# Optimization experiments

Measured on AMD Instinct MI355X. Metric: run time of the kernel, lower is better.

The kernel has to match this reference:

```python
import jax, jax.numpy as jnp
import numpy as np

H = 512   # hidden_size
B = 32    # batch
S = 2048  # src_len
NEG = -1e10


def setup_inputs() -> dict:
    key = jax.random.key(0)
    k1, k2, k3, k4, k5, k6 = jax.random.split(key, 6)
    hidden = jax.random.normal(k1, (B, 2 * H), dtype=jnp.float32)
    encoder_outputs = jax.random.normal(k2, (S, B, 2 * H), dtype=jnp.float32)
    mask = jax.random.randint(k3, (B, S), 0, 2, dtype=jnp.int32)
    # params: nn.Linear(4H, H) -> weight [H, 4H], bias [H]; v ~ U[0,1) [H]
    bound = 1.0 / np.sqrt(4 * H)
    attn_w = jax.random.uniform(k4, (H, 4 * H), minval=-bound, maxval=bound, dtype=jnp.float32)
    attn_b = jax.random.uniform(k5, (H,), minval=-bound, maxval=bound, dtype=jnp.float32)
    v = jax.random.uniform(k6, (H,), dtype=jnp.float32)
    return {"hidden": hidden, "encoder_outputs": encoder_outputs, "mask": mask,
            "attn_w": attn_w, "attn_b": attn_b, "v": v}


def reference(hidden, encoder_outputs, mask, attn_w, attn_b, v):
    # hidden: [B, 2H] -> [B, S, 2H]; encoder_outputs: [S, B, 2H] -> [B, S, 2H]
    src_len = encoder_outputs.shape[0]
    h = jnp.broadcast_to(hidden[:, None, :], (hidden.shape[0], src_len, hidden.shape[1]))
    eo = jnp.transpose(encoder_outputs, (1, 0, 2))
    cat = jnp.concatenate((h, eo), axis=2)                      # [B, S, 4H]
    energy = jnp.tanh(jnp.einsum('bsf,hf->bsh', cat, attn_w) + attn_b)  # [B, S, H]
    attention = jnp.einsum('bsh,h->bs', energy, v)              # [B, S]
    attention = jnp.where(mask == 0, NEG, attention)
    return jax.nn.softmax(attention, axis=1)
```

## Files before the change

kernel.cpp:

```cpp
#include <hip/hip_runtime.h>

#define SLEN 2048
#define BATCH 32
#define HDIM 512
#define KDIM 1024

typedef _Float16 f16x8 __attribute__((ext_vector_type(8)));
typedef _Float16 f16x4 __attribute__((ext_vector_type(4)));
typedef float f32x4 __attribute__((ext_vector_type(4)));

__device__ __forceinline__ void gload16(const void* g, void* l) {
  __builtin_amdgcn_global_load_lds(
      (const __attribute__((address_space(1))) unsigned int*)g,
      (__attribute__((address_space(3))) unsigned int*)l, 16, 0, 0);
}

__device__ __forceinline__ float fast_tanh(float x) {
  float e = __expf(2.0f * x);
  return 1.0f - 2.0f * __builtin_amdgcn_rcpf(e + 1.0f);
}

__global__ __launch_bounds__(256) void prep_k(const float* __restrict__ attn_w,
                                              const float* __restrict__ attn_b,
                                              const float* __restrict__ hidden,
                                              _Float16* __restrict__ Bt,
                                              float* __restrict__ s1,
                                              float* __restrict__ score) {
  if (blockIdx.x < 512) {
    int t = blockIdx.x * 256 + threadIdx.x;
    int h = t >> 8;
    int c = t & 255;
    float4 x = *(const float4*)(attn_w + (size_t)h * 2048 + 1024 + c * 4);
    f16x4 y = {(_Float16)x.x, (_Float16)x.y, (_Float16)x.z, (_Float16)x.w};
    *(f16x4*)(Bt + (size_t)h * 1024 + c * 4) = y;
  } else if (blockIdx.x < 4608) {
    int o = (blockIdx.x - 512) * 4 + (threadIdx.x >> 6);
    int b = o >> 9, h = o & 511;
    int lane = threadIdx.x & 63;
    const float4* hp = (const float4*)(hidden + (size_t)b * 1024);
    const float4* wp = (const float4*)(attn_w + (size_t)h * 2048);
    float acc = 0.f;
#pragma unroll
    for (int c = 0; c < 4; ++c) {
      float4 a = hp[c * 64 + lane];
      float4 wv = wp[c * 64 + lane];
      acc += a.x * wv.x + a.y * wv.y + a.z * wv.z + a.w * wv.w;
    }
#pragma unroll
    for (int off = 1; off < 64; off <<= 1) acc += __shfl_xor(acc, off);
    if (lane == 0) s1[o] = acc + attn_b[h];
  } else {
    int idx = (blockIdx.x - 4608) * 256 + threadIdx.x;
    float4 z = {0.f, 0.f, 0.f, 0.f};
    ((float4*)score)[idx] = z;
    ((float4*)score)[idx + 8192] = z;
  }
}

__global__ __launch_bounds__(256, 2) void gemm_k(const float* __restrict__ eo,
                                                 const _Float16* __restrict__ Bt,
                                                 const float* __restrict__ s1,
                                                 const float* __restrict__ v,
                                                 float* __restrict__ score) {
  constexpr int BK = 64;
  __shared__ __align__(16) float As[256 * BK];
  __shared__ __align__(16) _Float16 Bs[128 * BK];

  int bid = blockIdx.x;
  int x = bid & 7;
  int q = bid >> 3;
  int nt = q & 3;
  int mt = (q >> 2) * 8 + x;

  int tid = threadIdx.x;
  int lane = tid & 63;
  int w = tid >> 6;
  int wm = w * 64;

  const float* ga[8];
  const _Float16* gb[4];
#pragma unroll
  for (int ii = 0; ii < 8; ++ii) {
    int iss = w * 16 + ii;
    int rloc = iss * 4 + (lane >> 4);
    int sc = (lane & 15) ^ (rloc & 15);
    ga[ii] = eo + (size_t)(mt * 256 + rloc) * KDIM + sc * 4;
  }
#pragma unroll
  for (int ii = 0; ii < 4; ++ii) {
    int iss = w * 4 + ii;
    int rloc = iss * 8 + (lane >> 3);
    int sc = (lane & 7) ^ (rloc & 7);
    gb[ii] = Bt + (size_t)(nt * 128 + rloc) * KDIM + sc * 8;
  }

  f32x4 acc[4][8];
#pragma unroll
  for (int i = 0; i < 4; ++i)
#pragma unroll
    for (int j = 0; j < 8; ++j) acc[i][j] = (f32x4){0.f, 0.f, 0.f, 0.f};

  int mrow = lane & 15;
  int quad = lane >> 4;
  for (int kt = 0; kt < KDIM / BK; ++kt) {
    __syncthreads();
#pragma unroll
    for (int ii = 0; ii < 8; ++ii) {
      gload16(ga[ii], (char*)As + (w * 16 + ii) * 1024);
      gload16(ga[ii] + 32 * KDIM, (char*)As + (w * 16 + ii + 8) * 1024);
      ga[ii] += BK;
    }
#pragma unroll
    for (int ii = 0; ii < 4; ++ii) {
      gload16(gb[ii], (char*)Bs + (w * 4 + ii) * 1024);
      gb[ii] += BK;
    }
    __syncthreads();

#pragma unroll
    for (int kk = 0; kk < 2; ++kk) {
      int c0 = kk * 8 + quad * 2;
      int cB = kk * 4 + quad;
      f16x8 af[4], bf[8];
#pragma unroll
      for (int j = 0; j < 8; ++j)
        bf[j] = *(const f16x8*)&Bs[(16 * j + mrow) * BK + ((cB ^ (mrow & 7)) << 3)];
#pragma unroll
      for (int i = 0; i < 4; ++i) {
        const float* pa = &As[(wm + 16 * i + mrow) * BK];
        float4 a0 = *(const float4*)(pa + ((c0 ^ mrow) << 2));
        float4 a1 = *(const float4*)(pa + (((c0 + 1) ^ mrow) << 2));
        f16x8 t = {(_Float16)a0.x, (_Float16)a0.y, (_Float16)a0.z, (_Float16)a0.w,
                   (_Float16)a1.x, (_Float16)a1.y, (_Float16)a1.z, (_Float16)a1.w};
        af[i] = t;
      }
#pragma unroll
      for (int i = 0; i < 4; ++i)
#pragma unroll
        for (int j = 0; j < 8; ++j)
          acc[i][j] = __builtin_amdgcn_mfma_f32_16x16x32_f16(af[i], bf[j], acc[i][j], 0, 0, 0);
    }
  }

  __syncthreads();
  float* s1s = (float*)As;
  float* vsm = (float*)Bs;
  for (int t = tid; t < 1024; t += 256) {
    int bb = t >> 5, cc = t & 31;
    ((float4*)s1s)[bb * 33 + cc] = *(const float4*)(s1 + (size_t)bb * 512 + nt * 128 + cc * 4);
  }
  if (tid < 32) ((float4*)vsm)[tid] = *(const float4*)(v + nt * 128 + tid * 4);
  __syncthreads();

  int lcol = lane & 15;
  float vv[8];
#pragma unroll
  for (int j = 0; j < 8; ++j) vv[j] = vsm[16 * j + lcol];

#pragma unroll
  for (int i = 0; i < 4; ++i) {
#pragma unroll
    for (int r = 0; r < 4; ++r) {
      int mloc = wm + 16 * i + 4 * quad + r;
      int bb = mloc & 31;
      float sum = 0.f;
#pragma unroll
      for (int j = 0; j < 8; ++j) {
        float e = acc[i][j][r] + s1s[bb * 132 + 16 * j + lcol];
        sum += fast_tanh(e) * vv[j];
      }
      sum += __shfl_xor(sum, 1);
      sum += __shfl_xor(sum, 2);
      sum += __shfl_xor(sum, 4);
      sum += __shfl_xor(sum, 8);
      if (lcol == 0) {
        int mg = mt * 256 + mloc;
        atomicAdd(&score[(mg & 31) * SLEN + (mg >> 5)], sum);
      }
    }
  }
}

__global__ __launch_bounds__(256) void softmax_k(const float* __restrict__ score,
                                                 const int* __restrict__ mask,
                                                 float* __restrict__ out) {
  int b = blockIdx.x;
  int tid = threadIdx.x;
  int lane = tid & 63, w = tid >> 6;
  __shared__ float red[8];
  float vals[8];
  float mx = -3.4e38f;
#pragma unroll
  for (int i = 0; i < 8; ++i) {
    int s = i * 256 + tid;
    float xv = score[b * SLEN + s];
    if (mask[b * SLEN + s] == 0) xv = -1e10f;
    vals[i] = xv;
    mx = fmaxf(mx, xv);
  }
#pragma unroll
  for (int off = 1; off < 64; off <<= 1) mx = fmaxf(mx, __shfl_xor(mx, off));
  if (lane == 0) red[w] = mx;
  __syncthreads();
  mx = fmaxf(fmaxf(red[0], red[1]), fmaxf(red[2], red[3]));
  float sum = 0.f;
#pragma unroll
  for (int i = 0; i < 8; ++i) {
    vals[i] = __expf(vals[i] - mx);
    sum += vals[i];
  }
#pragma unroll
  for (int off = 1; off < 64; off <<= 1) sum += __shfl_xor(sum, off);
  if (lane == 0) red[4 + w] = sum;
  __syncthreads();
  sum = red[4] + red[5] + red[6] + red[7];
  float inv = 1.0f / sum;
#pragma unroll
  for (int i = 0; i < 8; ++i) out[b * SLEN + i * 256 + tid] = vals[i] * inv;
}

extern "C" void kernel_launch(void* const* d_in, const int* in_sizes, int n_in,
                              void* d_out, int out_size, void* d_ws, size_t ws_size,
                              hipStream_t stream) {
  const float* hidden = (const float*)d_in[0];
  const float* eo     = (const float*)d_in[1];
  const int*   mask   = (const int*)d_in[2];
  const float* attn_w = (const float*)d_in[3];
  const float* attn_b = (const float*)d_in[4];
  const float* v      = (const float*)d_in[5];
  float* out = (float*)d_out;

  char* wsb = (char*)d_ws;
  _Float16* Bt = (_Float16*)wsb;
  float* s1    = (float*)(wsb + (1 << 20));
  float* score = (float*)(wsb + (1 << 20) + (1 << 16));

  prep_k<<<4640, 256, 0, stream>>>(attn_w, attn_b, hidden, Bt, s1, score);
  gemm_k<<<1024, 256, 0, stream>>>(eo, Bt, s1, v, score);
  softmax_k<<<BATCH, 256, 0, stream>>>(score, mask, out);
}
```

Baseline: 441.2 us.

## Double-buffer GEMM LDS tiles with BK=32 and prefetch the next K tile

Halves the K tile to 32 and keeps two LDS buffers for A and B. The next tile's global-to-LDS loads are issued before the MFMAs on the current tile run, so load latency can overlap compute, and the loop needs one barrier per iteration instead of two. Address swizzles are rebuilt for the narrower tile, and `s_setprio` raises wave priority around the MFMA block. Total LDS use stays about the same. The overlap may be lost if the compiler inserts conservative vmcnt waits before the LDS reads, and the smaller K step doubles the number of loop iterations and barriers.

```diff
diff --git a/kernel.cpp b/kernel.cpp
--- a/kernel.cpp
+++ b/kernel.cpp
@@ -62,9 +62,10 @@
                                                  const float* __restrict__ s1,
                                                  const float* __restrict__ v,
                                                  float* __restrict__ score) {
-  constexpr int BK = 64;
-  __shared__ __align__(16) float As[256 * BK];
-  __shared__ __align__(16) _Float16 Bs[128 * BK];
+  constexpr int BK = 32;
+  constexpr int NKT = KDIM / BK;
+  __shared__ __align__(16) float As[2][256 * BK];
+  __shared__ __align__(16) _Float16 Bs[2][128 * BK];
 
   int bid = blockIdx.x;
   int x = bid & 7;
@@ -78,21 +79,14 @@
   int wm = w * 64;
 
   const float* ga[8];
-  const _Float16* gb[4];
-#pragma unroll
-  for (int ii = 0; ii < 8; ++ii) {
-    int iss = w * 16 + ii;
-    int rloc = iss * 4 + (lane >> 4);
-    int sc = (lane & 15) ^ (rloc & 15);
-    ga[ii] = eo + (size_t)(mt * 256 + rloc) * KDIM + sc * 4;
-  }
-#pragma unroll
-  for (int ii = 0; ii < 4; ++ii) {
-    int iss = w * 4 + ii;
-    int rloc = iss * 8 + (lane >> 3);
-    int sc = (lane & 7) ^ (rloc & 7);
-    gb[ii] = Bt + (size_t)(nt * 128 + rloc) * KDIM + sc * 8;
-  }
+  const _Float16* gb[2];
+#pragma unroll
+  for (int i = 0; i < 8; ++i)
+    ga[i] = eo + (size_t)(mt * 256 + 64 * w + 8 * i + (lane >> 3)) * KDIM
+              + (((lane & 7) ^ (lane >> 3)) << 2);
+  gb[0] = Bt + (size_t)(nt * 128 + 32 * w + (lane >> 2)) * KDIM
+            + (((lane & 3) ^ (lane >> 4)) << 3);
+  gb[1] = gb[0] + 16 * KDIM;
 
   f32x4 acc[4][8];
 #pragma unroll
@@ -102,44 +96,57 @@
 
   int mrow = lane & 15;
   int quad = lane >> 4;
-  for (int kt = 0; kt < KDIM / BK; ++kt) {
+  int bchunk = (quad ^ (mrow >> 2)) & 3;
+  int as_sw = mrow & 7;
+
+  {
+    gload16(gb[0], (char*)Bs[0] + (w * 2 + 0) * 1024);
+    gload16(gb[1], (char*)Bs[0] + (w * 2 + 1) * 1024);
+    gb[0] += BK; gb[1] += BK;
+#pragma unroll
+    for (int i = 0; i < 8; ++i) {
+      gload16(ga[i], (char*)As[0] + (w * 8 + i) * 1024);
+      ga[i] += BK;
+    }
+  }
+
+  for (int kt = 0; kt < NKT; ++kt) {
+    int cur = kt & 1;
     __syncthreads();
-#pragma unroll
-    for (int ii = 0; ii < 8; ++ii) {
-      gload16(ga[ii], (char*)As + (w * 16 + ii) * 1024);
-      gload16(ga[ii] + 32 * KDIM, (char*)As + (w * 16 + ii + 8) * 1024);
-      ga[ii] += BK;
-    }
-#pragma unroll
-    for (int ii = 0; ii < 4; ++ii) {
-      gload16(gb[ii], (char*)Bs + (w * 4 + ii) * 1024);
-      gb[ii] += BK;
-    }
-    __syncthreads();
-
-#pragma unroll
-    for (int kk = 0; kk < 2; ++kk) {
-      int c0 = kk * 8 + quad * 2;
-      int cB = kk * 4 + quad;
-      f16x8 af[4], bf[8];
+
+    if (kt + 1 < NKT) {
+      gload16(gb[0], (char*)Bs[cur ^ 1] + (w * 2 + 0) * 1024);
+      gload16(gb[1], (char*)Bs[cur ^ 1] + (w * 2 + 1) * 1024);
+      gb[0] += BK; gb[1] += BK;
+#pragma unroll
+      for (int i = 0; i < 8; ++i) {
+        gload16(ga[i], (char*)As[cur ^ 1] + (w * 8 + i) * 1024);
+        ga[i] += BK;
+      }
+    }
+
+    const float* Ab = As[cur];
+    const _Float16* Bb = Bs[cur];
+    f16x8 bf[8], af[4];
+#pragma unroll
+    for (int j = 0; j < 8; ++j)
+      bf[j] = *(const f16x8*)&Bb[(16 * j + mrow) * BK + (bchunk << 3)];
+#pragma unroll
+    for (int i = 0; i < 4; ++i) {
+      const float* pa = &Ab[(wm + 16 * i + mrow) * BK];
+      float4 a0 = *(const float4*)(pa + (((2 * quad) ^ as_sw) << 2));
+      float4 a1 = *(const float4*)(pa + (((2 * quad + 1) ^ as_sw) << 2));
+      f16x8 t = {(_Float16)a0.x, (_Float16)a0.y, (_Float16)a0.z, (_Float16)a0.w,
+                 (_Float16)a1.x, (_Float16)a1.y, (_Float16)a1.z, (_Float16)a1.w};
+      af[i] = t;
+    }
+    __builtin_amdgcn_s_setprio(1);
+#pragma unroll
+    for (int i = 0; i < 4; ++i)
 #pragma unroll
       for (int j = 0; j < 8; ++j)
-        bf[j] = *(const f16x8*)&Bs[(16 * j + mrow) * BK + ((cB ^ (mrow & 7)) << 3)];
-#pragma unroll
-      for (int i = 0; i < 4; ++i) {
-        const float* pa = &As[(wm + 16 * i + mrow) * BK];
-        float4 a0 = *(const float4*)(pa + ((c0 ^ mrow) << 2));
-        float4 a1 = *(const float4*)(pa + (((c0 + 1) ^ mrow) << 2));
-        f16x8 t = {(_Float16)a0.x, (_Float16)a0.y, (_Float16)a0.z, (_Float16)a0.w,
-                   (_Float16)a1.x, (_Float16)a1.y, (_Float16)a1.z, (_Float16)a1.w};
-        af[i] = t;
-      }
-#pragma unroll
-      for (int i = 0; i < 4; ++i)
-#pragma unroll
-        for (int j = 0; j < 8; ++j)
-          acc[i][j] = __builtin_amdgcn_mfma_f32_16x16x32_f16(af[i], bf[j], acc[i][j], 0, 0, 0);
-    }
+        acc[i][j] = __builtin_amdgcn_mfma_f32_16x16x32_f16(af[i], bf[j], acc[i][j], 0, 0, 0);
+    __builtin_amdgcn_s_setprio(0);
   }
 
   __syncthreads();
```

New measurement: 439.0 us. No clear change (-0.5%).

## Load A fragments directly from global and stage B halves in large LDS buffer

Applied to the files above, without the earlier changes.

The GEMM kernel now uses 512-thread blocks covering 512 rows by 128 columns. It stages the fp16 weight tile for half of K (512 columns) into a 128KB LDS buffer with XOR swizzling. Encoder-output rows are read straight from global into registers and converted to fp16, which drops the async global-to-LDS copies of the fp32 A tile and most of the per-K-step barriers. In exchange, A loads lose LDS sharing and coalescing and must hide their latency through unrolling. The 128KB of LDS per block with launch_bounds(512,2) also constrains occupancy.

```diff
diff --git a/kernel.cpp b/kernel.cpp
--- a/kernel.cpp
+++ b/kernel.cpp
@@ -8,12 +8,6 @@
 typedef _Float16 f16x8 __attribute__((ext_vector_type(8)));
 typedef _Float16 f16x4 __attribute__((ext_vector_type(4)));
 typedef float f32x4 __attribute__((ext_vector_type(4)));
-
-__device__ __forceinline__ void gload16(const void* g, void* l) {
-  __builtin_amdgcn_global_load_lds(
-      (const __attribute__((address_space(1))) unsigned int*)g,
-      (__attribute__((address_space(3))) unsigned int*)l, 16, 0, 0);
-}
 
 __device__ __forceinline__ float fast_tanh(float x) {
   float e = __expf(2.0f * x);
@@ -57,83 +51,83 @@
   }
 }
 
-__global__ __launch_bounds__(256, 2) void gemm_k(const float* __restrict__ eo,
+__global__ __launch_bounds__(512, 2) void gemm_k(const float* __restrict__ eo,
                                                  const _Float16* __restrict__ Bt,
                                                  const float* __restrict__ s1,
                                                  const float* __restrict__ v,
                                                  float* __restrict__ score) {
-  constexpr int BK = 64;
-  __shared__ __align__(16) float As[256 * BK];
-  __shared__ __align__(16) _Float16 Bs[128 * BK];
+  __shared__ __align__(16) char smem[131072];
 
   int bid = blockIdx.x;
   int x = bid & 7;
-  int q = bid >> 3;
-  int nt = q & 3;
-  int mt = (q >> 2) * 8 + x;
+  int nt = (bid >> 3) & 3;
+  int mt = (bid >> 5) * 8 + x;
 
   int tid = threadIdx.x;
   int lane = tid & 63;
   int w = tid >> 6;
   int wm = w * 64;
-
-  const float* ga[8];
-  const _Float16* gb[4];
-#pragma unroll
-  for (int ii = 0; ii < 8; ++ii) {
-    int iss = w * 16 + ii;
-    int rloc = iss * 4 + (lane >> 4);
-    int sc = (lane & 15) ^ (rloc & 15);
-    ga[ii] = eo + (size_t)(mt * 256 + rloc) * KDIM + sc * 4;
-  }
-#pragma unroll
-  for (int ii = 0; ii < 4; ++ii) {
-    int iss = w * 4 + ii;
-    int rloc = iss * 8 + (lane >> 3);
-    int sc = (lane & 7) ^ (rloc & 7);
-    gb[ii] = Bt + (size_t)(nt * 128 + rloc) * KDIM + sc * 8;
-  }
-
-  f32x4 acc[4][8];
-#pragma unroll
-  for (int i = 0; i < 4; ++i)
-#pragma unroll
-    for (int j = 0; j < 8; ++j) acc[i][j] = (f32x4){0.f, 0.f, 0.f, 0.f};
-
   int mrow = lane & 15;
   int quad = lane >> 4;
-  for (int kt = 0; kt < KDIM / BK; ++kt) {
+  int rk = mrow & 7;
+
+  f32x4 acc[4][8];
+#pragma unroll
+  for (int i = 0; i < 4; ++i)
+#pragma unroll
+    for (int j = 0; j < 8; ++j) acc[i][j] = (f32x4){0.f, 0.f, 0.f, 0.f};
+
+#pragma unroll 1
+  for (int half = 0; half < 2; ++half) {
+    int h0 = half * 512;
+
     __syncthreads();
-#pragma unroll
-    for (int ii = 0; ii < 8; ++ii) {
-      gload16(ga[ii], (char*)As + (w * 16 + ii) * 1024);
-      gload16(ga[ii] + 32 * KDIM, (char*)As + (w * 16 + ii + 8) * 1024);
-      ga[ii] += BK;
-    }
-#pragma unroll
-    for (int ii = 0; ii < 4; ++ii) {
-      gload16(gb[ii], (char*)Bs + (w * 4 + ii) * 1024);
-      gb[ii] += BK;
+    {
+      int r = tid >> 2;
+      int cg = (tid & 3) * 16;
+      const _Float16* src = Bt + (size_t)(nt * 128 + r) * 1024 + h0 + cg * 8;
+      char* dst = smem + r * 1024;
+#pragma unroll
+      for (int c = 0; c < 16; ++c) {
+        f16x8 vd = *(const f16x8*)(src + c * 8);
+        int pc = (cg + c) ^ (r & 7);
+        *(f16x8*)(dst + pc * 16) = vd;
+      }
     }
     __syncthreads();
 
-#pragma unroll
-    for (int kk = 0; kk < 2; ++kk) {
-      int c0 = kk * 8 + quad * 2;
-      int cB = kk * 4 + quad;
-      f16x8 af[4], bf[8];
+    const float* aB0 = eo + (size_t)(mt * 512 + wm + 0  + mrow) * 1024 + h0 + quad * 8;
+    const float* aB1 = eo + (size_t)(mt * 512 + wm + 16 + mrow) * 1024 + h0 + quad * 8;
+    const float* aB2 = eo + (size_t)(mt * 512 + wm + 32 + mrow) * 1024 + h0 + quad * 8;
+    const float* aB3 = eo + (size_t)(mt * 512 + wm + 48 + mrow) * 1024 + h0 + quad * 8;
+
+#pragma unroll 2
+    for (int ks = 0; ks < 16; ++ks) {
+      float4 ar0 = *(const float4*)(aB0 + ks * 32);
+      float4 ar1 = *(const float4*)(aB0 + ks * 32 + 4);
+      float4 ar2 = *(const float4*)(aB1 + ks * 32);
+      float4 ar3 = *(const float4*)(aB1 + ks * 32 + 4);
+      float4 ar4 = *(const float4*)(aB2 + ks * 32);
+      float4 ar5 = *(const float4*)(aB2 + ks * 32 + 4);
+      float4 ar6 = *(const float4*)(aB3 + ks * 32);
+      float4 ar7 = *(const float4*)(aB3 + ks * 32 + 4);
+
+      int cx = ((ks * 4 + quad) ^ rk) << 4;
+      f16x8 bf[8];
 #pragma unroll
       for (int j = 0; j < 8; ++j)
-        bf[j] = *(const f16x8*)&Bs[(16 * j + mrow) * BK + ((cB ^ (mrow & 7)) << 3)];
-#pragma unroll
-      for (int i = 0; i < 4; ++i) {
-        const float* pa = &As[(wm + 16 * i + mrow) * BK];
-        float4 a0 = *(const float4*)(pa + ((c0 ^ mrow) << 2));
-        float4 a1 = *(const float4*)(pa + (((c0 + 1) ^ mrow) << 2));
-        f16x8 t = {(_Float16)a0.x, (_Float16)a0.y, (_Float16)a0.z, (_Float16)a0.w,
-                   (_Float16)a1.x, (_Float16)a1.y, (_Float16)a1.z, (_Float16)a1.w};
-        af[i] = t;
-      }
+        bf[j] = *(const f16x8*)(smem + ((16 * j + mrow) << 10) + cx);
+
+      f16x8 af[4];
+      af[0] = (f16x8){(_Float16)ar0.x, (_Float16)ar0.y, (_Float16)ar0.z, (_Float16)ar0.w,
+                      (_Float16)ar1.x, (_Float16)ar1.y, (_Float16)ar1.z, (_Float16)ar1.w};
+      af[1] = (f16x8){(_Float16)ar2.x, (_Float16)ar2.y, (_Float16)ar2.z, (_Float16)ar2.w,
+                      (_Float16)ar3.x, (_Float16)ar3.y, (_Float16)ar3.z, (_Float16)ar3.w};
+      af[2] = (f16x8){(_Float16)ar4.x, (_Float16)ar4.y, (_Float16)ar4.z, (_Float16)ar4.w,
+                      (_Float16)ar5.x, (_Float16)ar5.y, (_Float16)ar5.z, (_Float16)ar5.w};
+      af[3] = (f16x8){(_Float16)ar6.x, (_Float16)ar6.y, (_Float16)ar6.z, (_Float16)ar6.w,
+                      (_Float16)ar7.x, (_Float16)ar7.y, (_Float16)ar7.z, (_Float16)ar7.w};
+
 #pragma unroll
       for (int i = 0; i < 4; ++i)
 #pragma unroll
@@ -143,16 +137,16 @@
   }
 
   __syncthreads();
-  float* s1s = (float*)As;
-  float* vsm = (float*)Bs;
-  for (int t = tid; t < 1024; t += 256) {
+  float* s1s = (float*)smem;
+  float* vsm = (float*)(smem + 16896);
+  for (int t = tid; t < 1024; t += 512) {
     int bb = t >> 5, cc = t & 31;
     ((float4*)s1s)[bb * 33 + cc] = *(const float4*)(s1 + (size_t)bb * 512 + nt * 128 + cc * 4);
   }
   if (tid < 32) ((float4*)vsm)[tid] = *(const float4*)(v + nt * 128 + tid * 4);
   __syncthreads();
 
-  int lcol = lane & 15;
+  int lcol = mrow;
   float vv[8];
 #pragma unroll
   for (int j = 0; j < 8; ++j) vv[j] = vsm[16 * j + lcol];
@@ -174,7 +168,7 @@
       sum += __shfl_xor(sum, 4);
       sum += __shfl_xor(sum, 8);
       if (lcol == 0) {
-        int mg = mt * 256 + mloc;
+        int mg = mt * 512 + mloc;
         atomicAdd(&score[(mg & 31) * SLEN + (mg >> 5)], sum);
       }
     }
@@ -236,6 +230,6 @@
   float* score = (float*)(wsb + (1 << 20) + (1 << 16));
 
   prep_k<<<4640, 256, 0, stream>>>(attn_w, attn_b, hidden, Bt, s1, score);
-  gemm_k<<<1024, 256, 0, stream>>>(eo, Bt, s1, v, score);
+  gemm_k<<<512, 512, 0, stream>>>(eo, Bt, s1, v, score);
   softmax_k<<<BATCH, 256, 0, stream>>>(score, mask, out);
 }
```

New measurement: 527.5 us. +19.5%, slower.
